# Kernel tuning notes

Hardware: AMD Instinct MI355X
Metric: run time of the kernel (lower is better)

Reference implementation:

```python
import jax, jax.numpy as jnp
import numpy as np

K = 5  # kernel_size per dim
# 2^dim = 4 active degree-1 B-spline products per edge (dim=2)
BITS = jnp.array([[0, 0], [1, 0], [0, 1], [1, 1]], dtype=jnp.int32)  # [S,2]


def spline_basis(edge_attr):
    """Open B-spline basis, degree=1, dim=2, kernel_size=5 per dim.
    Returns basis weights [E,S] and flattened kernel indices [E,S]."""
    v = edge_attr * (K - 1)                 # scale pseudo-coords to knot grid
    i0 = jnp.floor(v)
    f = v - i0                              # fractional part, [E,2]
    # per-dim linear weights: f for bit=1, (1-f) for bit=0
    w = jnp.where(BITS[None] == 1, f[:, None, :], 1.0 - f[:, None, :])  # [E,S,2]
    basis = w[..., 0] * w[..., 1]           # [E,S]
    idx = jnp.minimum(i0.astype(jnp.int32)[:, None, :] + BITS[None], K - 1)  # [E,S,2]
    kidx = idx[..., 0] + K * idx[..., 1]    # flatten 2D kernel index -> [0,25)
    return basis, kidx


def spline_conv(x, src, dst, basis, kidx, W, root, bias, n):
    # transform-then-gather: y[n,k,:] = x[n] @ W[k]
    y = jnp.einsum('ni,kio->nko', x, W)                 # [N,25,out]
    g = y[src[:, None], kidx]                           # gather [E,S,out]
    msg = jnp.einsum('es,eso->eo', basis, g)            # weighted sum over S
    agg = jax.ops.segment_sum(msg, dst, num_segments=n)  # scatter-add to targets
    return agg + x @ root + bias                        # root weight + bias


def setup_inputs() -> dict:
    key = jax.random.key(0)
    ks = jax.random.split(key, 8)
    N, E, IN, H, OUT = 50000, 400000, 32, 64, 64
    x = jax.random.normal(ks[0], (N, IN), jnp.float32)
    edge_index = jax.random.randint(ks[1], (2, E), 0, N, dtype=jnp.int32)
    edge_attr = jax.random.uniform(ks[2], (E, 2), jnp.float32)

    def glorot(k, shape):
        fan = shape[-2] + shape[-1]
        return jax.random.normal(k, shape, jnp.float32) * jnp.sqrt(2.0 / fan)

    W1 = glorot(ks[3], (K * K, IN, H));  root1 = glorot(ks[4], (IN, H));  b1 = jnp.zeros((H,), jnp.float32)
    W2 = glorot(ks[5], (K * K, H, OUT)); root2 = glorot(ks[6], (H, OUT)); b2 = jnp.zeros((OUT,), jnp.float32)
    fc_w = glorot(ks[7], (OUT, 3));      fc_b = jnp.zeros((3,), jnp.float32)
    return dict(x=x, edge_index=edge_index, edge_attr=edge_attr,
                W1=W1, root1=root1, b1=b1, W2=W2, root2=root2, b2=b2,
                fc_w=fc_w, fc_b=fc_b)


def reference(x, edge_index, edge_attr, W1, root1, b1, W2, root2, b2, fc_w, fc_b):
    # eval-mode forward (dropout is identity at inference)
    n = x.shape[0]
    src, dst = edge_index[0], edge_index[1]
    basis, kidx = spline_basis(edge_attr)
    h = jax.nn.relu(spline_conv(x, src, dst, basis, kidx, W1, root1, b1, n))
    h = jax.nn.relu(spline_conv(h, src, dst, basis, kidx, W2, root2, b2, n))
    return h @ fc_w + fc_b
```

## Files before the change

### kernel.cpp

```cpp
#include <hip/hip_runtime.h>
#include <stdint.h>

typedef __attribute__((ext_vector_type(8))) short short8;
typedef __attribute__((ext_vector_type(4))) float f32x4;
typedef __attribute__((ext_vector_type(4))) unsigned short ushort4v;

__device__ __forceinline__ unsigned short f2bf(float f) {
    unsigned int u = __float_as_uint(f);
    u = (u + 0x7FFFu + ((u >> 16) & 1u)) >> 16;
    return (unsigned short)u;
}
__device__ __forceinline__ float bf2f(unsigned short h) {
    return __uint_as_float(((unsigned int)h) << 16);
}
__device__ __forceinline__ int cell_of(float ax, float ay) {
    int c0 = (int)floorf(ax * 4.f); c0 = min(max(c0, 0), 3);
    int c1 = (int)floorf(ay * 4.f); c1 = min(max(c1, 0), 3);
    return c0 + 4 * c1;
}

template<int KIN>
__device__ __forceinline__ void pack_cell_elem(const float* __restrict__ W,
                                               unsigned short* __restrict__ pkc, int u) {
    constexpr int KCH = KIN / 8;
    if (u >= 16 * 4 * KCH * 512) return;
    int low9 = u & 511;
    int grp  = u >> 9;
    int kc = grp % KCH; grp /= KCH;
    int c  = grp & 3;
    int cell = grp >> 2;
    int lane = low9 >> 3, j = low9 & 7;
    int k = kc * 32 + (lane >> 4) * 8 + j;
    int t = k / KIN, i = k % KIN;
    int k0 = (cell & 3) + (t & 1);   if (k0 > 4) k0 = 4;
    int k1 = (cell >> 2) + (t >> 1); if (k1 > 4) k1 = 4;
    float val = W[((size_t)(k0 + 5 * k1) * KIN + i) * 64 + (c * 16 + (lane & 15))];
    pkc[u] = f2bf(val);
}

template<int KIN>
__device__ __forceinline__ void pack_root_elem(const float* __restrict__ root,
                                               unsigned short* __restrict__ pkr, int u) {
    constexpr int KCHr = KIN / 32;
    if (u >= 4 * KCHr * 512) return;
    int low9 = u & 511;
    int grp  = u >> 9;
    int lane = low9 >> 3, j = low9 & 7;
    int kc = grp % KCHr, c = grp / KCHr;
    int k = kc * 32 + (lane >> 4) * 8 + j;
    int o = c * 16 + (lane & 15);
    float v = root[(size_t)k * 64 + o];
    unsigned short h = f2bf(v);
    pkr[(size_t)(grp * 2) * 512 + low9]     = h;
    pkr[(size_t)(grp * 2 + 1) * 512 + low9] = f2bf(v - bf2f(h));
}

__global__ __launch_bounds__(256) void prep_kernel(
    const float* __restrict__ attr, const int* __restrict__ dst,
    int* __restrict__ hist, int* __restrict__ dhist, int E,
    const float* __restrict__ W1, const float* __restrict__ W2,
    const float* __restrict__ root1, const float* __restrict__ root2,
    unsigned short* __restrict__ pkc1, unsigned short* __restrict__ pkc2,
    unsigned short* __restrict__ pkr1, unsigned short* __restrict__ pkr2,
    const float* __restrict__ x, unsigned short* __restrict__ xb, int n4,
    int EB)
{
    __shared__ int wcnt[4][16];
    int b = blockIdx.x;
    if (b < EB) {
        int e = b * 256 + threadIdx.x;
        int lane = threadIdx.x & 63, wave = threadIdx.x >> 6;
        int cell = -1;
        if (e < E) {
            float2 a = reinterpret_cast<const float2*>(attr)[e];
            cell = cell_of(a.x, a.y);
            atomicAdd(&dhist[dst[e]], 1);
        }
        #pragma unroll
        for (int c = 0; c < 16; c++) {
            unsigned long long m = __ballot(cell == c);
            if (lane == 0) wcnt[wave][c] = __popcll(m);
        }
        __syncthreads();
        if (threadIdx.x < 16) {
            int c = threadIdx.x;
            int tot = wcnt[0][c] + wcnt[1][c] + wcnt[2][c] + wcnt[3][c];
            if (tot) atomicAdd(&hist[c], tot);
        }
        return;
    }
    b -= EB;
    if (b < 512)  { pack_cell_elem<32>(W1, pkc1, b * 256 + threadIdx.x); return; }
    b -= 512;
    if (b < 1024) { pack_cell_elem<64>(W2, pkc2, b * 256 + threadIdx.x); return; }
    b -= 1024;
    if (b < 8)    { pack_root_elem<32>(root1, pkr1, b * 256 + threadIdx.x); return; }
    b -= 8;
    if (b < 16)   { pack_root_elem<64>(root2, pkr2, b * 256 + threadIdx.x); return; }
    b -= 16;
    {
        int t = b * 256 + threadIdx.x;
        if (t < n4) {
            float4 v = reinterpret_cast<const float4*>(x)[t];
            ushort4v o = { f2bf(v.x), f2bf(v.y), f2bf(v.z), f2bf(v.w) };
            reinterpret_cast<ushort4v*>(xb)[t] = o;
        }
    }
}

__global__ __launch_bounds__(1024) void scanA_kernel(const int* __restrict__ dhist,
                                                     int* __restrict__ nof,
                                                     int* __restrict__ bsum, int Np1) {
    __shared__ int wsum[16];
    int tid = threadIdx.x, lane = tid & 63, w = tid >> 6;
    int i = blockIdx.x * 1024 + tid;
    int v = (i < Np1) ? dhist[i] : 0;
    int s = v;
    #pragma unroll
    for (int off = 1; off < 64; off <<= 1) {
        int t = __shfl_up(s, off);
        if (lane >= off) s += t;
    }
    if (lane == 63) wsum[w] = s;
    __syncthreads();
    if (tid == 0) {
        int a = 0;
        #pragma unroll
        for (int k = 0; k < 16; k++) { int t = wsum[k]; wsum[k] = a; a += t; }
        bsum[blockIdx.x] = a;
    }
    __syncthreads();
    if (i < Np1) nof[i] = wsum[w] + s - v;
}

__global__ void scan_small_kernel(const int* __restrict__ hist, int* __restrict__ off_e,
                                  int* __restrict__ off_b, int* __restrict__ cursor,
                                  const int* __restrict__ bsum, int* __restrict__ bbase, int NB) {
    if (threadIdx.x == 0 && blockIdx.x == 0) {
        int se = 0, sb = 0;
        for (int c = 0; c < 16; c++) {
            off_e[c] = se; off_b[c] = sb; cursor[c] = se;
            se += hist[c]; sb += (hist[c] + 63) >> 6;
        }
        off_e[16] = se; off_b[16] = sb;
        int a = 0;
        for (int bks = 0; bks < NB; bks++) { int t = bsum[bks]; bbase[bks] = a; a += t; }
    }
}

__global__ __launch_bounds__(256) void scatter_kernel(const float* __restrict__ attr,
                                                      const int* __restrict__ dst,
                                                      const int* __restrict__ nof,
                                                      const int* __restrict__ bbase,
                                                      int* __restrict__ bucket,
                                                      int* __restrict__ cursor,
                                                      int* __restrict__ cursor_d,
                                                      int* __restrict__ dstpos, int E) {
    __shared__ int wcnt[4][16];
    __shared__ int wbase[4][16];
    int e = blockIdx.x * 256 + threadIdx.x;
    int lane = threadIdx.x & 63, wave = threadIdx.x >> 6;
    int cell = -1;
    if (e < E) {
        float2 a = reinterpret_cast<const float2*>(attr)[e];
        cell = cell_of(a.x, a.y);
        int d = dst[e];
        dstpos[e] = nof[d] + bbase[d >> 10] + atomicAdd(&cursor_d[d], 1);
    }
    int myrank = 0;
    #pragma unroll
    for (int c = 0; c < 16; c++) {
        unsigned long long m = __ballot(cell == c);
        if (cell == c) myrank = __popcll(m & ((1ull << lane) - 1ull));
        if (lane == 0) wcnt[wave][c] = __popcll(m);
    }
    __syncthreads();
    if (threadIdx.x < 16) {
        int c = threadIdx.x;
        int t0 = wcnt[0][c], t1 = wcnt[1][c], t2 = wcnt[2][c], t3 = wcnt[3][c];
        int tot = t0 + t1 + t2 + t3;
        int g = tot ? atomicAdd(&cursor[c], tot) : 0;
        wbase[0][c] = g;
        wbase[1][c] = g + t0;
        wbase[2][c] = g + t0 + t1;
        wbase[3][c] = g + t0 + t1 + t2;
    }
    __syncthreads();
    if (e < E) bucket[wbase[wave][cell] + myrank] = e;
}

template<int KIN>
__global__ __launch_bounds__(256) void root_gemm_kernel(
    const unsigned short* __restrict__ Xb, const unsigned short* __restrict__ pkr,
    float* __restrict__ rt, const float* __restrict__ bias, int N)
{
    constexpr int KCHr = KIN / 32;
    const int lane = threadIdx.x & 63;
    const int wave = threadIdx.x >> 6;
    const int lrow = lane & 15, lch = lane >> 4;
    const int mbase = blockIdx.x * 64 + wave * 16;

    short8 afrag[KCHr];
    {
        int row = mbase + lrow;
        if (row > N - 1) row = N - 1;
        const unsigned short* ap = Xb + (size_t)row * KIN + lch * 8;
        #pragma unroll
        for (int kc = 0; kc < KCHr; kc++)
            afrag[kc] = *reinterpret_cast<const short8*>(ap + kc * 32);
    }
    f32x4 acc[4];
    #pragma unroll
    for (int c = 0; c < 4; c++) acc[c] = (f32x4){0.f, 0.f, 0.f, 0.f};
    #pragma unroll
    for (int c = 0; c < 4; c++) {
        #pragma unroll
        for (int kc = 0; kc < KCHr; kc++) {
            short8 bh = *reinterpret_cast<const short8*>(pkr + ((size_t)(c * KCHr + kc) * 2    ) * 512 + lane * 8);
            short8 bl = *reinterpret_cast<const short8*>(pkr + ((size_t)(c * KCHr + kc) * 2 + 1) * 512 + lane * 8);
            acc[c] = __builtin_amdgcn_mfma_f32_16x16x32_bf16(afrag[kc], bh, acc[c], 0, 0, 0);
            acc[c] = __builtin_amdgcn_mfma_f32_16x16x32_bf16(afrag[kc], bl, acc[c], 0, 0, 0);
        }
    }
    #pragma unroll
    for (int c = 0; c < 4; c++) {
        int o = c * 16 + lrow;
        float bv = bias[o];
        #pragma unroll
        for (int r = 0; r < 4; r++) {
            int m = mbase + lch * 4 + r;
            if (m < N) rt[(size_t)m * 64 + o] = acc[c][r] + bv;
        }
    }
}

template<int KIN>
__global__ __launch_bounds__(256) void edge_gemm_kernel(
    const unsigned short* __restrict__ Xb,
    const unsigned short* __restrict__ pkc,
    float* __restrict__ msg,
    const int* __restrict__ src,
    const float* __restrict__ attr, const int* __restrict__ bucket,
    const int* __restrict__ dstpos,
    const int* __restrict__ off_e, const int* __restrict__ off_b)
{
    constexpr int KCHr = KIN / 32;
    constexpr int KCH  = 4 * KCHr;
    __shared__ unsigned short Blds[4 * KCH * 512];

    const int b = blockIdx.x;
    if (b >= off_b[16]) return;
    int cell = 0;
    #pragma unroll
    for (int c = 1; c < 16; c++) cell += (b >= off_b[c]);
    const int tile = b - off_b[cell];

    {
        const short8* sp = reinterpret_cast<const short8*>(pkc + (size_t)cell * (4 * KCH * 512));
        short8* dp = reinterpret_cast<short8*>(Blds);
        #pragma unroll
        for (int p = 0; p < (4 * KCH * 512 / 8) / 256; p++)
            dp[p * 256 + threadIdx.x] = sp[p * 256 + threadIdx.x];
    }

    const int lane = threadIdx.x & 63;
    const int wave = threadIdx.x >> 6;
    const int lrow = lane & 15, lch = lane >> 4;

    const int ebeg = off_e[cell];
    const int eend = off_e[cell + 1];
    const int eslot = ebeg + (tile * 4 + wave) * 16 + lrow;
    const bool valid = eslot < eend;

    int eid = 0, s = 0, mp = -1;
    float ax = 0.f, ay = 0.f;
    if (valid) {
        eid = bucket[eslot];
        s = src[eid];
        mp = dstpos[eid];
        float2 a = reinterpret_cast<const float2*>(attr)[eid];
        ax = a.x; ay = a.y;
    }
    const float f0 = ax * 4.f - (float)(cell & 3);
    const float f1 = ay * 4.f - (float)(cell >> 2);
    float w[4] = { (1.f - f0) * (1.f - f1), f0 * (1.f - f1),
                   (1.f - f0) * f1,         f0 * f1 };

    short8 xfrag[KCHr];
    {
        const unsigned short* xp = Xb + (size_t)s * KIN + lch * 8;
        #pragma unroll
        for (int kcr = 0; kcr < KCHr; kcr++)
            xfrag[kcr] = *reinterpret_cast<const short8*>(xp + kcr * 32);
    }

    float wr[4][4];
    int pv[4];
    #pragma unroll
    for (int r = 0; r < 4; r++) {
        int er = lch * 4 + r;
        #pragma unroll
        for (int t = 0; t < 4; t++) wr[t][r] = __shfl(w[t], er);
        pv[r] = __shfl(mp, er);
    }

    __syncthreads();

    #pragma unroll
    for (int ch = 0; ch < 2; ch++) {
        f32x4 accT[4][2];
        #pragma unroll
        for (int t = 0; t < 4; t++)
            #pragma unroll
            for (int c2 = 0; c2 < 2; c2++)
                accT[t][c2] = (f32x4){0.f, 0.f, 0.f, 0.f};

        #pragma unroll
        for (int t = 0; t < 4; t++) {
            #pragma unroll
            for (int kcr = 0; kcr < KCHr; kcr++) {
                #pragma unroll
                for (int c2 = 0; c2 < 2; c2++) {
                    int c = ch * 2 + c2;
                    short8 bf = *reinterpret_cast<const short8*>(
                        &Blds[(size_t)((c * KCH) + (t * KCHr + kcr)) * 512 + lane * 8]);
                    accT[t][c2] = __builtin_amdgcn_mfma_f32_16x16x32_bf16(xfrag[kcr], bf, accT[t][c2], 0, 0, 0);
                }
            }
        }

        #pragma unroll
        for (int c2 = 0; c2 < 2; c2++) {
            const int o = (ch * 2 + c2) * 16 + lrow;
            #pragma unroll
            for (int r = 0; r < 4; r++) {
                if (pv[r] >= 0) {
                    float m = wr[0][r] * accT[0][c2][r] + wr[1][r] * accT[1][c2][r]
                            + wr[2][r] * accT[2][c2][r] + wr[3][r] * accT[3][c2][r];
                    msg[(size_t)pv[r] * 64 + o] = m;
                }
            }
        }
    }
}

template<int MODE>
__global__ __launch_bounds__(256) void segsum_kernel(
    const float* __restrict__ msg, const float* __restrict__ rt,
    const int* __restrict__ nof, const int* __restrict__ bbase,
    unsigned short* __restrict__ hout,
    const float* __restrict__ fcw, const float* __restrict__ fcb,
    float* __restrict__ out, int N)
{
    int n = blockIdx.x * 4 + (threadIdx.x >> 6);
    if (n >= N) return;
    int lane = threadIdx.x & 63;
    float acc = rt[(size_t)n * 64 + lane];
    int jb = nof[n]     + bbase[n >> 10];
    int je = nof[n + 1] + bbase[(n + 1) >> 10];
    int j = jb;
    for (; j + 1 < je; j += 2) {
        float a0 = msg[(size_t)j * 64 + lane];
        float a1 = msg[(size_t)(j + 1) * 64 + lane];
        acc += a0; acc += a1;
    }
    if (j < je) acc += msg[(size_t)j * 64 + lane];
    acc = fmaxf(acc, 0.f);
    if (MODE == 0) {
        hout[(size_t)n * 64 + lane] = f2bf(acc);
    } else {
        float p0 = acc * fcw[lane * 3 + 0];
        float p1 = acc * fcw[lane * 3 + 1];
        float p2 = acc * fcw[lane * 3 + 2];
        #pragma unroll
        for (int off = 32; off; off >>= 1) {
            p0 += __shfl_xor(p0, off);
            p1 += __shfl_xor(p1, off);
            p2 += __shfl_xor(p2, off);
        }
        if (lane == 0) {
            out[(size_t)n * 3 + 0] = p0 + fcb[0];
            out[(size_t)n * 3 + 1] = p1 + fcb[1];
            out[(size_t)n * 3 + 2] = p2 + fcb[2];
        }
    }
}

extern "C" void kernel_launch(void* const* d_in, const int* in_sizes, int n_in,
                              void* d_out, int out_size, void* d_ws, size_t ws_size,
                              hipStream_t stream)
{
    const float* x     = (const float*)d_in[0];
    const int*   ei    = (const int*)  d_in[1];
    const float* attr  = (const float*)d_in[2];
    const float* W1    = (const float*)d_in[3];
    const float* root1 = (const float*)d_in[4];
    const float* b1    = (const float*)d_in[5];
    const float* W2    = (const float*)d_in[6];
    const float* root2 = (const float*)d_in[7];
    const float* b2    = (const float*)d_in[8];
    const float* fcw   = (const float*)d_in[9];
    const float* fcb   = (const float*)d_in[10];

    const int N = in_sizes[0] / 32;
    const int E = in_sizes[1] / 2;
    const int* srcp = ei;
    const int* dstp = ei + E;

    char* wsp = (char*)d_ws;
    auto alloc = [&](size_t bytes) -> char* {
        char* p = wsp;
        wsp += (bytes + 255) & ~(size_t)255;
        return p;
    };
    const int NB = (N + 1 + 1023) / 1024;

    float*          rt       = (float*)alloc((size_t)N * 64 * 4);
    unsigned short* xb       = (unsigned short*)alloc((size_t)N * 32 * 2);
    unsigned short* h1b      = (unsigned short*)alloc((size_t)N * 64 * 2);
    unsigned short* pkr1     = (unsigned short*)alloc((size_t)4 * 1 * 2 * 512 * 2);
    unsigned short* pkr2     = (unsigned short*)alloc((size_t)4 * 2 * 2 * 512 * 2);
    unsigned short* pkc1     = (unsigned short*)alloc((size_t)16 * 4 * 4 * 512 * 2);
    unsigned short* pkc2     = (unsigned short*)alloc((size_t)16 * 4 * 8 * 512 * 2);
    int*            bucket   = (int*)alloc((size_t)E * 4);
    int*            dstpos   = (int*)alloc((size_t)E * 4);
    int*            nof      = (int*)alloc((size_t)(N + 1) * 4);
    int*            bsum     = (int*)alloc((size_t)NB * 4);
    int*            bbase    = (int*)alloc((size_t)NB * 4);
    int*            off_e    = (int*)alloc(17 * 4);
    int*            off_b    = (int*)alloc(17 * 4);
    int*            cursor   = (int*)alloc(16 * 4);
    int*            zbase    = (int*)alloc((size_t)(16 + (N + 1) + N) * 4);
    int*            hist     = zbase;
    int*            dhist    = zbase + 16;
    int*            cursor_d = zbase + 16 + (N + 1);
    float*          msg      = (float*)alloc((size_t)E * 64 * 4);

    hipMemsetAsync(zbase, 0, (size_t)(16 + (N + 1) + N) * 4, stream);

    const int EB = (E + 255) / 256;
    const int CB = (N * 8 + 255) / 256;
    const int prep_grid = EB + 512 + 1024 + 8 + 16 + CB;

    prep_kernel<<<prep_grid, 256, 0, stream>>>(attr, dstp, hist, dhist, E,
                                               W1, W2, root1, root2,
                                               pkc1, pkc2, pkr1, pkr2,
                                               x, xb, N * 8, EB);
    scanA_kernel<<<NB, 1024, 0, stream>>>(dhist, nof, bsum, N + 1);
    scan_small_kernel<<<1, 64, 0, stream>>>(hist, off_e, off_b, cursor, bsum, bbase, NB);
    scatter_kernel<<<EB, 256, 0, stream>>>(attr, dstp, nof, bbase, bucket, cursor, cursor_d, dstpos, E);

    const int egrid = (E + 63) / 64 + 16;
    const int sgrid = (N + 3) / 4;

    root_gemm_kernel<32><<<(N + 63) / 64, 256, 0, stream>>>(xb, pkr1, rt, b1, N);
    edge_gemm_kernel<32><<<egrid, 256, 0, stream>>>(xb, pkc1, msg, srcp, attr, bucket, dstpos, off_e, off_b);
    segsum_kernel<0><<<sgrid, 256, 0, stream>>>(msg, rt, nof, bbase, h1b, fcw, fcb, (float*)d_out, N);

    root_gemm_kernel<64><<<(N + 63) / 64, 256, 0, stream>>>(h1b, pkr2, rt, b2, N);
    edge_gemm_kernel<64><<<egrid, 256, 0, stream>>>(h1b, pkc2, msg, srcp, attr, bucket, dstpos, off_e, off_b);
    segsum_kernel<1><<<sgrid, 256, 0, stream>>>(msg, rt, nof, bbase, nullptr, fcw, fcb, (float*)d_out, N);
}
```

Before: 214.3 us.

## Store edge messages in bf16, merge root and edge GEMMs, reuse dst histogram

Edge messages are now written and read as bf16 instead of fp32, halving the traffic of the E×64 intermediate between the edge GEMM and segment-sum kernels. The root GEMM and edge GEMM are merged into one launch that splits its blocks by index, which cuts launches and lets the two parts overlap. The per-destination cursor array is removed by atomically decrementing the degree histogram to get ranks, and the memset becomes a small zero kernel. bf16 rounding of messages before accumulation adds precision error.

```diff
diff --git a/kernel.cpp b/kernel.cpp
--- a/kernel.cpp
+++ b/kernel.cpp
@@ -17,6 +17,11 @@
     int c0 = (int)floorf(ax * 4.f); c0 = min(max(c0, 0), 3);
     int c1 = (int)floorf(ay * 4.f); c1 = min(max(c1, 0), 3);
     return c0 + 4 * c1;
+}
+
+__global__ __launch_bounds__(256) void zero_kernel(int* __restrict__ p, int n) {
+    int t = blockIdx.x * 256 + threadIdx.x;
+    if (t < n) p[t] = 0;
 }
 
 template<int KIN>
@@ -154,7 +159,7 @@
                                                       const int* __restrict__ bbase,
                                                       int* __restrict__ bucket,
                                                       int* __restrict__ cursor,
-                                                      int* __restrict__ cursor_d,
+                                                      int* __restrict__ dhist,
                                                       int* __restrict__ dstpos, int E) {
     __shared__ int wcnt[4][16];
     __shared__ int wbase[4][16];
@@ -165,7 +170,8 @@
         float2 a = reinterpret_cast<const float2*>(attr)[e];
         cell = cell_of(a.x, a.y);
         int d = dst[e];
-        dstpos[e] = nof[d] + bbase[d >> 10] + atomicAdd(&cursor_d[d], 1);
+        int rank = atomicSub(&dhist[d], 1) - 1;
+        dstpos[e] = nof[d] + bbase[d >> 10] + rank;
     }
     int myrank = 0;
     #pragma unroll
@@ -190,65 +196,61 @@
 }
 
 template<int KIN>
-__global__ __launch_bounds__(256) void root_gemm_kernel(
-    const unsigned short* __restrict__ Xb, const unsigned short* __restrict__ pkr,
-    float* __restrict__ rt, const float* __restrict__ bias, int N)
-{
-    constexpr int KCHr = KIN / 32;
-    const int lane = threadIdx.x & 63;
-    const int wave = threadIdx.x >> 6;
-    const int lrow = lane & 15, lch = lane >> 4;
-    const int mbase = blockIdx.x * 64 + wave * 16;
-
-    short8 afrag[KCHr];
-    {
-        int row = mbase + lrow;
-        if (row > N - 1) row = N - 1;
-        const unsigned short* ap = Xb + (size_t)row * KIN + lch * 8;
-        #pragma unroll
-        for (int kc = 0; kc < KCHr; kc++)
-            afrag[kc] = *reinterpret_cast<const short8*>(ap + kc * 32);
-    }
-    f32x4 acc[4];
-    #pragma unroll
-    for (int c = 0; c < 4; c++) acc[c] = (f32x4){0.f, 0.f, 0.f, 0.f};
-    #pragma unroll
-    for (int c = 0; c < 4; c++) {
-        #pragma unroll
-        for (int kc = 0; kc < KCHr; kc++) {
-            short8 bh = *reinterpret_cast<const short8*>(pkr + ((size_t)(c * KCHr + kc) * 2    ) * 512 + lane * 8);
-            short8 bl = *reinterpret_cast<const short8*>(pkr + ((size_t)(c * KCHr + kc) * 2 + 1) * 512 + lane * 8);
-            acc[c] = __builtin_amdgcn_mfma_f32_16x16x32_bf16(afrag[kc], bh, acc[c], 0, 0, 0);
-            acc[c] = __builtin_amdgcn_mfma_f32_16x16x32_bf16(afrag[kc], bl, acc[c], 0, 0, 0);
-        }
-    }
-    #pragma unroll
-    for (int c = 0; c < 4; c++) {
-        int o = c * 16 + lrow;
-        float bv = bias[o];
-        #pragma unroll
-        for (int r = 0; r < 4; r++) {
-            int m = mbase + lch * 4 + r;
-            if (m < N) rt[(size_t)m * 64 + o] = acc[c][r] + bv;
-        }
-    }
-}
-
-template<int KIN>
-__global__ __launch_bounds__(256) void edge_gemm_kernel(
+__global__ __launch_bounds__(256) void layer_kernel(
     const unsigned short* __restrict__ Xb,
-    const unsigned short* __restrict__ pkc,
-    float* __restrict__ msg,
-    const int* __restrict__ src,
-    const float* __restrict__ attr, const int* __restrict__ bucket,
-    const int* __restrict__ dstpos,
+    const unsigned short* __restrict__ pkr, float* __restrict__ rt,
+    const float* __restrict__ bias, int N, int RG,
+    const unsigned short* __restrict__ pkc, unsigned short* __restrict__ msg,
+    const int* __restrict__ src, const float* __restrict__ attr,
+    const int* __restrict__ bucket, const int* __restrict__ dstpos,
     const int* __restrict__ off_e, const int* __restrict__ off_b)
 {
     constexpr int KCHr = KIN / 32;
     constexpr int KCH  = 4 * KCHr;
     __shared__ unsigned short Blds[4 * KCH * 512];
 
-    const int b = blockIdx.x;
+    const int lane = threadIdx.x & 63;
+    const int wave = threadIdx.x >> 6;
+    const int lrow = lane & 15, lch = lane >> 4;
+
+    if (blockIdx.x < RG) {
+        const int mbase = blockIdx.x * 64 + wave * 16;
+        short8 afrag[KCHr];
+        {
+            int row = mbase + lrow;
+            if (row > N - 1) row = N - 1;
+            const unsigned short* ap = Xb + (size_t)row * KIN + lch * 8;
+            #pragma unroll
+            for (int kc = 0; kc < KCHr; kc++)
+                afrag[kc] = *reinterpret_cast<const short8*>(ap + kc * 32);
+        }
+        f32x4 acc[4];
+        #pragma unroll
+        for (int c = 0; c < 4; c++) acc[c] = (f32x4){0.f, 0.f, 0.f, 0.f};
+        #pragma unroll
+        for (int c = 0; c < 4; c++) {
+            #pragma unroll
+            for (int kc = 0; kc < KCHr; kc++) {
+                short8 bh = *reinterpret_cast<const short8*>(pkr + ((size_t)(c * KCHr + kc) * 2    ) * 512 + lane * 8);
+                short8 bl = *reinterpret_cast<const short8*>(pkr + ((size_t)(c * KCHr + kc) * 2 + 1) * 512 + lane * 8);
+                acc[c] = __builtin_amdgcn_mfma_f32_16x16x32_bf16(afrag[kc], bh, acc[c], 0, 0, 0);
+                acc[c] = __builtin_amdgcn_mfma_f32_16x16x32_bf16(afrag[kc], bl, acc[c], 0, 0, 0);
+            }
+        }
+        #pragma unroll
+        for (int c = 0; c < 4; c++) {
+            int o = c * 16 + lrow;
+            float bv = bias[o];
+            #pragma unroll
+            for (int r = 0; r < 4; r++) {
+                int m = mbase + lch * 4 + r;
+                if (m < N) rt[(size_t)m * 64 + o] = acc[c][r] + bv;
+            }
+        }
+        return;
+    }
+
+    const int b = blockIdx.x - RG;
     if (b >= off_b[16]) return;
     int cell = 0;
     #pragma unroll
@@ -262,10 +264,6 @@
         for (int p = 0; p < (4 * KCH * 512 / 8) / 256; p++)
             dp[p * 256 + threadIdx.x] = sp[p * 256 + threadIdx.x];
     }
-
-    const int lane = threadIdx.x & 63;
-    const int wave = threadIdx.x >> 6;
-    const int lrow = lane & 15, lch = lane >> 4;
 
     const int ebeg = off_e[cell];
     const int eend = off_e[cell + 1];
@@ -337,7 +335,7 @@
                 if (pv[r] >= 0) {
                     float m = wr[0][r] * accT[0][c2][r] + wr[1][r] * accT[1][c2][r]
                             + wr[2][r] * accT[2][c2][r] + wr[3][r] * accT[3][c2][r];
-                    msg[(size_t)pv[r] * 64 + o] = m;
+                    msg[(size_t)pv[r] * 64 + o] = f2bf(m);
                 }
             }
         }
@@ -346,7 +344,7 @@
 
 template<int MODE>
 __global__ __launch_bounds__(256) void segsum_kernel(
-    const float* __restrict__ msg, const float* __restrict__ rt,
+    const unsigned short* __restrict__ msg, const float* __restrict__ rt,
     const int* __restrict__ nof, const int* __restrict__ bbase,
     unsigned short* __restrict__ hout,
     const float* __restrict__ fcw, const float* __restrict__ fcb,
@@ -359,12 +357,14 @@
     int jb = nof[n]     + bbase[n >> 10];
     int je = nof[n + 1] + bbase[(n + 1) >> 10];
     int j = jb;
-    for (; j + 1 < je; j += 2) {
-        float a0 = msg[(size_t)j * 64 + lane];
-        float a1 = msg[(size_t)(j + 1) * 64 + lane];
-        acc += a0; acc += a1;
-    }
-    if (j < je) acc += msg[(size_t)j * 64 + lane];
+    for (; j + 3 < je; j += 4) {
+        float a0 = bf2f(msg[(size_t)(j + 0) * 64 + lane]);
+        float a1 = bf2f(msg[(size_t)(j + 1) * 64 + lane]);
+        float a2 = bf2f(msg[(size_t)(j + 2) * 64 + lane]);
+        float a3 = bf2f(msg[(size_t)(j + 3) * 64 + lane]);
+        acc += a0; acc += a1; acc += a2; acc += a3;
+    }
+    for (; j < je; j++) acc += bf2f(msg[(size_t)j * 64 + lane]);
     acc = fmaxf(acc, 0.f);
     if (MODE == 0) {
         hout[(size_t)n * 64 + lane] = f2bf(acc);
@@ -430,13 +430,13 @@
     int*            off_e    = (int*)alloc(17 * 4);
     int*            off_b    = (int*)alloc(17 * 4);
     int*            cursor   = (int*)alloc(16 * 4);
-    int*            zbase    = (int*)alloc((size_t)(16 + (N + 1) + N) * 4);
+    int*            zbase    = (int*)alloc((size_t)(16 + N + 1) * 4);
     int*            hist     = zbase;
     int*            dhist    = zbase + 16;
-    int*            cursor_d = zbase + 16 + (N + 1);
-    float*          msg      = (float*)alloc((size_t)E * 64 * 4);
-
-    hipMemsetAsync(zbase, 0, (size_t)(16 + (N + 1) + N) * 4, stream);
+    unsigned short* msg      = (unsigned short*)alloc((size_t)E * 64 * 2);
+
+    const int ZN = 16 + N + 1;
+    zero_kernel<<<(ZN + 255) / 256, 256, 0, stream>>>(zbase, ZN);
 
     const int EB = (E + 255) / 256;
     const int CB = (N * 8 + 255) / 256;
@@ -448,16 +448,17 @@
                                                x, xb, N * 8, EB);
     scanA_kernel<<<NB, 1024, 0, stream>>>(dhist, nof, bsum, N + 1);
     scan_small_kernel<<<1, 64, 0, stream>>>(hist, off_e, off_b, cursor, bsum, bbase, NB);
-    scatter_kernel<<<EB, 256, 0, stream>>>(attr, dstp, nof, bbase, bucket, cursor, cursor_d, dstpos, E);
-
-    const int egrid = (E + 63) / 64 + 16;
+    scatter_kernel<<<EB, 256, 0, stream>>>(attr, dstp, nof, bbase, bucket, cursor, dhist, dstpos, E);
+
+    const int RG = (N + 63) / 64;
+    const int lgrid = RG + (E + 63) / 64 + 16;
     const int sgrid = (N + 3) / 4;
 
-    root_gemm_kernel<32><<<(N + 63) / 64, 256, 0, stream>>>(xb, pkr1, rt, b1, N);
-    edge_gemm_kernel<32><<<egrid, 256, 0, stream>>>(xb, pkc1, msg, srcp, attr, bucket, dstpos, off_e, off_b);
+    layer_kernel<32><<<lgrid, 256, 0, stream>>>(xb, pkr1, rt, b1, N, RG,
+                                                pkc1, msg, srcp, attr, bucket, dstpos, off_e, off_b);
     segsum_kernel<0><<<sgrid, 256, 0, stream>>>(msg, rt, nof, bbase, h1b, fcw, fcb, (float*)d_out, N);
 
-    root_gemm_kernel<64><<<(N + 63) / 64, 256, 0, stream>>>(h1b, pkr2, rt, b2, N);
-    edge_gemm_kernel<64><<<egrid, 256, 0, stream>>>(h1b, pkc2, msg, srcp, attr, bucket, dstpos, off_e, off_b);
+    layer_kernel<64><<<lgrid, 256, 0, stream>>>(h1b, pkr2, rt, b2, N, RG,
+                                                pkc2, msg, srcp, attr, bucket, dstpos, off_e, off_b);
     segsum_kernel<1><<<sgrid, 256, 0, stream>>>(msg, rt, nof, bbase, nullptr, fcw, fcb, (float*)d_out, N);
 }
```

Measured after the change: 187.4 us. 12.5% less time.
